# Performance work log

Measured on AMD Instinct MI355X. Metric: run time of the kernel, lower is better.

Reference implementation:

```python
import jax, jax.numpy as jnp
import numpy as np
from jax import lax

B, L = 16384, 32
HID, CIN = 8, 2
N_SUB = 2            # RK4 substeps per spline interval (fixed-step stand-in for torchcde's adaptive solver)
T10_LO, T10_HI = 0.1, 7.0


def push_zeros(a):
    # torch: move nonzero entries of each row to the right end, zeros to the left.
    # stable ascending sort on validity key (0 for zeros, 1 for valid) reproduces this exactly
    # because the invalid entries are exactly 0.
    keys = (a != 0).astype(jnp.int32)
    order = jnp.argsort(keys, axis=1)  # jax sorts are stable
    return jnp.take_along_axis(a, order, axis=1)


def setup_inputs() -> dict:
    key = jax.random.key(0)
    ks = jax.random.split(key, 12)
    fa_len = jax.random.randint(ks[0], (B, 1), L // 2, L + 1)          # 16..32 valid points
    valid = jnp.arange(L)[None, :] < fa_len                             # (B, L)
    X_fa_in = jnp.where(valid, jax.random.uniform(ks[1], (B, L), minval=0.1, maxval=1.1), 0.0)
    fa_vals_in = jnp.where(valid, jax.random.uniform(ks[2], (B, L), minval=0.05, maxval=0.45), 0.0)
    TR_vals = jax.random.uniform(ks[3], (B, 1), minval=0.003, maxval=0.01)
    fa_mask = valid

    def lin(k, fout, fin):
        kw, kb = jax.random.split(k)
        s = 1.0 / np.sqrt(fin)
        return (jax.random.uniform(kw, (fout, fin), minval=-s, maxval=s),
                jax.random.uniform(kb, (fout,), minval=-s, maxval=s))

    W_init, b_init = lin(ks[4], HID, CIN)        # self.initial: Linear(2, 8)
    W1, b1 = lin(ks[5], 256, HID)                # CDE_Func.linear1
    W2, b2 = lin(ks[6], CIN * HID, 256)          # CDE_Func.linear2
    Wr1, br1 = lin(ks[7], 200, HID)              # reg_T10
    Wr2, br2 = lin(ks[8], 200, 200)
    Wr3, br3 = lin(ks[9], 1, 200)
    return dict(X_fa_in=X_fa_in, fa_vals_in=fa_vals_in, TR_vals=TR_vals,
                W_init=W_init, b_init=b_init, W1=W1, b1=b1, W2=W2, b2=b2,
                Wr1=Wr1, br1=br1, Wr2=Wr2, br2=br2, Wr3=Wr3, br3=br3,
                fa_mask=fa_mask, fa_len=fa_len)


def _forward(X_fa_in, fa_vals_in, TR_vals, W_init, b_init, W1, b1, W2, b2,
             Wr1, br1, Wr2, br2, Wr3, br3, fa_mask, fa_len):
    fl = fa_len[:, 0]                       # (B,) int
    fl_f = fl.astype(X_fa_in.dtype)
    mean = jnp.sum(X_fa_in, axis=1) / fl_f
    Xn = X_fa_in / mean[:, None]
    X_fa = push_zeros(Xn)
    fa_vals = push_zeros(fa_vals_in)
    bidx = jnp.arange(X_fa.shape[0])
    last_X = X_fa[bidx, fl - 1][:, None]            # pushed array indexed at fa_len-1 (as in torch)
    last_fa = fa_vals_in[bidx, fl - 1][:, None]     # original array indexed at fa_len-1
    X_fa = jnp.where(X_fa == 0.0, last_X, X_fa)
    fa_vals = jnp.where(fa_vals == 0.0, last_fa, fa_vals)
    x = jnp.stack([fa_vals, X_fa], axis=-1)         # (B, L, 2): channels (fa, X)

    # Hermite cubic with backward differences, unit knot spacing t_i = i
    diffs = x[:, 1:] - x[:, :-1]                    # (B, L-1, C)
    m = jnp.concatenate([diffs[:, :1], diffs], axis=1)  # m_0 = fwd diff, m_i = backward diff
    X0s, X1s = x[:, :-1], x[:, 1:]                  # per-interval knot values (B, L-1, C)
    M0s, M1s = m[:, :-1], m[:, 1:]

    z0 = x[:, 0] @ W_init.T + b_init                # X.evaluate(interval[0]) == first knot

    def f(z):  # CDE vector field: (B, HID) -> (B, HID, CIN)
        h = jax.nn.relu(z @ W1.T + b1)
        g = jnp.tanh(h @ W2.T + b2)
        return g.reshape(z.shape[0], HID, CIN)

    hstep = 1.0 / N_SUB
    nI = x.shape[1] - 1
    intervals = jnp.repeat(jnp.arange(nI), N_SUB)
    s0s = jnp.tile(jnp.arange(N_SUB) * hstep, nI).astype(x.dtype)

    def step(z, ts):
        i, s0 = ts
        x0, x1 = X0s[:, i], X1s[:, i]
        m0, m1 = M0s[:, i], M1s[:, i]

        def dX(s):  # spline derivative dX/dt at local coord s in [0,1]
            s2 = s * s
            return ((6 * s2 - 6 * s) * x0 + (3 * s2 - 4 * s + 1) * m0 +
                    (-6 * s2 + 6 * s) * x1 + (3 * s2 - 2 * s) * m1)

        def F(s, zz):
            return jnp.einsum('bhc,bc->bh', f(zz), dX(s))

        k1 = F(s0, z)
        k2 = F(s0 + hstep / 2, z + 0.5 * hstep * k1)
        k3 = F(s0 + hstep / 2, z + 0.5 * hstep * k2)
        k4 = F(s0 + hstep, z + hstep * k3)
        return z + (hstep / 6) * (k1 + 2 * k2 + 2 * k3 + k4), None

    z_T, _ = lax.scan(step, z0, (intervals, s0s))

    h1 = jax.nn.gelu(z_T @ Wr1.T + br1, approximate=False)
    h2 = jax.nn.gelu(h1 @ Wr2.T + br2, approximate=False)
    t = (h2 @ Wr3.T + br3)[:, 0]
    T10 = T10_LO + jax.nn.sigmoid(t)[:, None] * (T10_HI - T10_LO)   # (B, 1)
    R1 = 1.0 / T10
    E = jnp.exp(-TR_vals * R1)                                      # (B, 1)
    X_out = (1 - E) * jnp.sin(fa_vals_in) / (1 - jnp.cos(fa_vals_in) * E)
    mean2 = jnp.sum(X_out, axis=1) / fl_f
    X_out = X_out / mean2[:, None]
    M0 = jnp.ones_like(T10)
    return X_out, T10, M0


def reference(X_fa_in, fa_vals_in, TR_vals, W_init, b_init, W1, b1, W2, b2,
              Wr1, br1, Wr2, br2, Wr3, br3, fa_mask, fa_len):
    return _forward(X_fa_in, fa_vals_in, TR_vals, W_init, b_init, W1, b1, W2, b2,
                    Wr1, br1, Wr2, br2, Wr3, br3, fa_mask, fa_len)
```

## Files before the change

kernel.cpp:

```cpp
#include <hip/hip_runtime.h>
#include <hip/hip_bf16.h>

#define B_ROWS 16384
#define L_SEQ  32

typedef _Float16 f16;
typedef __attribute__((ext_vector_type(8))) _Float16 f16x8;
typedef __attribute__((ext_vector_type(4))) float f32x4;
typedef __attribute__((ext_vector_type(4))) unsigned int u32x4;

__device__ __forceinline__ unsigned pkh(float a, float b) {
    return __builtin_bit_cast(unsigned, __builtin_amdgcn_cvt_pkrtz(a, b));
}
__device__ __forceinline__ float tanh_fast(float x) {
    float e = __expf(2.0f * x);
    float r = __builtin_amdgcn_rcpf(e + 1.0f);
    return fmaf(-2.0f, r, 1.0f);
}
__device__ __forceinline__ float gelu_exact(float x) {
    return 0.5f * x * (1.0f + erff(x * 0.70710678118654752440f));
}

__global__ __launch_bounds__(256, 1) void ode_kernel(
    const float* __restrict__ Xin, const float* __restrict__ Fin,
    const int*   __restrict__ fa_len,
    const float* __restrict__ Wi,  const float* __restrict__ bi,
    const float* __restrict__ W1g, const float* __restrict__ b1g,
    const float* __restrict__ W2g, const float* __restrict__ b2g,
    float* __restrict__ zT)
{
    __shared__ __align__(16) float xm[64 * 132];
#define XM(r_, i_, c_) xm[(r_) * 132 + (i_) * 4 + (c_)]

    const int tid = threadIdx.x;
    const int g16 = tid >> 4, sub = tid & 15;

    float mean_r[4]; int fl_r[4];
#pragma unroll
    for (int r = 0; r < 4; ++r) {
        const int row_l = g16 * 4 + r;
        const int row   = blockIdx.x * 64 + row_l;
        const float* Xr = Xin + row * L_SEQ;
        const float* Fr = Fin + row * L_SEQ;
        float xr0 = Xr[sub], xr1 = Xr[sub + 16];
        float fr0 = Fr[sub], fr1 = Fr[sub + 16];
        fl_r[r] = fa_len[row];
        float s = xr0 + xr1;
        s += __shfl_xor(s, 1, 16);
        s += __shfl_xor(s, 2, 16);
        s += __shfl_xor(s, 4, 16);
        s += __shfl_xor(s, 8, 16);
        mean_r[r] = s / (float)fl_r[r];
        XM(row_l, sub, 0)      = fr0; XM(row_l, sub, 1)      = xr0;
        XM(row_l, sub + 16, 0) = fr1; XM(row_l, sub + 16, 1) = xr1;
    }
    __syncthreads();

    float ff[4][2], xf[4][2];
#pragma unroll
    for (int r = 0; r < 4; ++r) {
        const int row_l = g16 * 4 + r;
        const int fl = fl_r[r];
        const float mean = mean_r[r];
        const int shift = L_SEQ - fl;
        int lsrc  = fl - 1 - shift;
        int lsrcC = lsrc < 0 ? 0 : lsrc;
        float lastX = (lsrc >= 0) ? (XM(row_l, lsrcC, 1) / mean) : 0.0f;
        float lastF = XM(row_l, fl - 1, 0);
#pragma unroll
        for (int u = 0; u < 2; ++u) {
            int p = sub + u * 16;
            int src = p - shift;
            int sc  = src < 0 ? 0 : src;
            float fraw = XM(row_l, sc, 0);
            float xraw = XM(row_l, sc, 1);
            ff[r][u] = (src >= 0) ? fraw : lastF;
            xf[r][u] = (src >= 0) ? (xraw / mean) : lastX;
        }
    }
    __syncthreads();
#pragma unroll
    for (int r = 0; r < 4; ++r) {
        const int row_l = g16 * 4 + r;
#pragma unroll
        for (int u = 0; u < 2; ++u) {
            int p = sub + u * 16;
            XM(row_l, p, 0) = ff[r][u];
            XM(row_l, p, 1) = xf[r][u];
        }
    }
    __syncthreads();
#pragma unroll
    for (int r = 0; r < 4; ++r) {
        const int row_l = g16 * 4 + r;
#pragma unroll
        for (int u = 0; u < 2; ++u) {
            int p = sub + u * 16;
            int qd = (p == 0) ? 1 : p;
            XM(row_l, p, 2) = XM(row_l, qd, 0) - XM(row_l, qd - 1, 0);
            XM(row_l, p, 3) = XM(row_l, qd, 1) - XM(row_l, qd - 1, 1);
        }
    }
    __syncthreads();

    const int wv   = tid >> 6;
    const int lane = tid & 63;
    const int n    = lane & 15;
    const int q    = lane >> 4;
    const int rowl = wv * 16 + n;
    const int rowg = blockIdx.x * 64 + rowl;

    u32x4 a1[16];
#pragma unroll
    for (int t = 0; t < 16; ++t) {
        const float* wr = W1g + (t * 16 + n) * 8 + (q < 2 ? q * 4 : 0);
        float4 w4 = *(const float4*)wr;
        float b1v = b1g[t * 16 + n];
        unsigned d0 = (q < 2) ? pkh(w4.x, w4.y) : (q == 2 ? pkh(b1v, 0.0f) : 0u);
        unsigned d1 = (q < 2) ? pkh(w4.z, w4.w) : 0u;
        a1[t] = (u32x4){d0, d1, 0u, 0u};
    }
    u32x4 a2[8];
#pragma unroll
    for (int kk = 0; kk < 8; ++kk) {
        const float* w2r = W2g + n * 256 + kk * 32 + 4 * q;
        float4 p0 = *(const float4*)(w2r);
        float4 p1 = *(const float4*)(w2r + 16);
        a2[kk] = (u32x4){pkh(p0.x, p0.y), pkh(p0.z, p0.w), pkh(p1.x, p1.y), pkh(p1.z, p1.w)};
    }
    f32x4 c2seed;
#pragma unroll
    for (int r = 0; r < 4; ++r) c2seed[r] = b2g[4 * q + r];

    float f0 = XM(rowl, 0, 0), X0 = XM(rowl, 0, 1);
    float z0 = fmaf(Wi[(2 * q) * 2], f0, fmaf(Wi[(2 * q) * 2 + 1], X0, bi[2 * q]));
    float z1 = fmaf(Wi[(2 * q + 1) * 2], f0, fmaf(Wi[(2 * q + 1) * 2 + 1], X0, bi[2 * q + 1]));

    const int bpi = (((q & 1) << 5) + n) << 2;
    const f32x4 zero4 = {0.f, 0.f, 0.f, 0.f};

    auto FEVAL = [&](float zza, float zzb, float d0c, float d1c, float& ko0, float& ko1) {
        unsigned myz = pkh(zza, zzb);
        int b0 = __builtin_amdgcn_ds_bpermute(bpi, (int)myz);
        int b1 = __builtin_amdgcn_ds_bpermute(bpi + 64, (int)myz);
        unsigned bz0 = (q < 2) ? (unsigned)b0 : (q == 2 ? 0x3C00u : 0u);
        unsigned bz1 = (q < 2) ? (unsigned)b1 : 0u;
        f16x8 bz = __builtin_bit_cast(f16x8, (u32x4){bz0, bz1, 0u, 0u});

        f32x4 c1[16];
#pragma unroll
        for (int t = 0; t < 16; ++t)
            c1[t] = __builtin_amdgcn_mfma_f32_16x16x32_f16(
                __builtin_bit_cast(f16x8, a1[t]), bz, zero4, 0, 0, 0);

        u32x4 hf[8];
#pragma unroll
        for (int kk = 0; kk < 8; ++kk) {
            float v0 = fmaxf(c1[2 * kk][0], 0.f),     v1 = fmaxf(c1[2 * kk][1], 0.f);
            float v2 = fmaxf(c1[2 * kk][2], 0.f),     v3 = fmaxf(c1[2 * kk][3], 0.f);
            float w0 = fmaxf(c1[2 * kk + 1][0], 0.f), w1 = fmaxf(c1[2 * kk + 1][1], 0.f);
            float w2 = fmaxf(c1[2 * kk + 1][2], 0.f), w3 = fmaxf(c1[2 * kk + 1][3], 0.f);
            hf[kk] = (u32x4){pkh(v0, v1), pkh(v2, v3), pkh(w0, w1), pkh(w2, w3)};
        }

        f32x4 c2a = c2seed, c2b = zero4;
#pragma unroll
        for (int kk = 0; kk < 4; ++kk) {
            c2a = __builtin_amdgcn_mfma_f32_16x16x32_f16(
                __builtin_bit_cast(f16x8, a2[kk]), __builtin_bit_cast(f16x8, hf[kk]), c2a, 0, 0, 0);
            c2b = __builtin_amdgcn_mfma_f32_16x16x32_f16(
                __builtin_bit_cast(f16x8, a2[kk + 4]), __builtin_bit_cast(f16x8, hf[kk + 4]), c2b, 0, 0, 0);
        }
        f32x4 G = c2a + c2b;

        float t0 = tanh_fast(G[0]), t1 = tanh_fast(G[1]);
        float t2 = tanh_fast(G[2]), t3 = tanh_fast(G[3]);
        ko0 = fmaf(t0, d0c, t1 * d1c);
        ko1 = fmaf(t2, d0c, t3 * d1c);
    };

#pragma unroll 1
    for (int i = 0; i < 31; ++i) {
        float4 P0 = *(const float4*)&XM(rowl, i, 0);
        float4 P1 = *(const float4*)&XM(rowl, i + 1, 0);
        float m0f = P0.z, m0X = P0.w, m1f = P1.z, m1X = P1.w;
        float df  = P0.x - P1.x, dXx = P0.y - P1.y;

        float d25f = fmaf(-1.125f, df,  fmaf(0.1875f, m0f, -0.3125f * m1f));
        float d25X = fmaf(-1.125f, dXx, fmaf(0.1875f, m0X, -0.3125f * m1X));
        float d50f = fmaf(-1.5f,   df,  fmaf(-0.25f,  m0f, -0.25f   * m1f));
        float d50X = fmaf(-1.5f,   dXx, fmaf(-0.25f,  m0X, -0.25f   * m1X));
        float d75f = fmaf(-1.125f, df,  fmaf(-0.3125f, m0f, 0.1875f * m1f));
        float d75X = fmaf(-1.125f, dXx, fmaf(-0.3125f, m0X, 0.1875f * m1X));

#pragma unroll 1
        for (int ssi = 0; ssi < 2; ++ssi) {
            float daf = ssi ? d50f : m0f,  daX = ssi ? d50X : m0X;
            float dbf = ssi ? d75f : d25f, dbX = ssi ? d75X : d25X;
            float ddf = ssi ? m1f  : d50f, ddX = ssi ? m1X  : d50X;

            float k1a, k1b, k2a, k2b, k3a, k3b, k4a, k4b, zza, zzb;
            FEVAL(z0, z1, daf, daX, k1a, k1b);
            zza = fmaf(0.25f, k1a, z0); zzb = fmaf(0.25f, k1b, z1);
            FEVAL(zza, zzb, dbf, dbX, k2a, k2b);
            zza = fmaf(0.25f, k2a, z0); zzb = fmaf(0.25f, k2b, z1);
            FEVAL(zza, zzb, dbf, dbX, k3a, k3b);
            zza = fmaf(0.5f, k3a, z0);  zzb = fmaf(0.5f, k3b, z1);
            FEVAL(zza, zzb, ddf, ddX, k4a, k4b);

            float ka = fmaf(2.f, k2a, k1a); ka = fmaf(2.f, k3a, ka);
            float kb = fmaf(2.f, k2b, k1b); kb = fmaf(2.f, k3b, kb);
            z0 = fmaf(1.f / 12.f, ka + k4a, z0);
            z1 = fmaf(1.f / 12.f, kb + k4b, z1);
        }
    }

    *(float2*)(zT + rowg * 8 + 2 * q) = make_float2(z0, z1);
#undef XM
}

__global__ __launch_bounds__(256) void readout_kernel(
    const float* __restrict__ zT,
    const float* __restrict__ Fin,
    const float* __restrict__ TRv,
    const int*   __restrict__ fa_len,
    const float* __restrict__ Wr1, const float* __restrict__ br1,
    const float* __restrict__ Wr2, const float* __restrict__ br2,
    const float* __restrict__ Wr3, const float* __restrict__ br3,
    float* __restrict__ out)
{
    __shared__ float h1s[32][200];
    __shared__ float w2s[40][200];
    const int tid = threadIdx.x;
    const int g = tid >> 3, sub = tid & 7;
    const int row = blockIdx.x * 32 + g;

    float4 za = *(const float4*)(zT + row * 8);
    float4 zb = *(const float4*)(zT + row * 8 + 4);

#pragma unroll 5
    for (int t = 0; t < 25; ++t) {
        int j = sub + 8 * t;
        const float* w = Wr1 + j * 8;
        float4 wa = *(const float4*)(w);
        float4 wb = *(const float4*)(w + 4);
        float acc = br1[j];
        acc = fmaf(wa.x, za.x, acc);
        acc = fmaf(wa.y, za.y, acc);
        acc = fmaf(wa.z, za.z, acc);
        acc = fmaf(wa.w, za.w, acc);
        acc = fmaf(wb.x, zb.x, acc);
        acc = fmaf(wb.y, zb.y, acc);
        acc = fmaf(wb.z, zb.z, acc);
        acc = fmaf(wb.w, zb.w, acc);
        h1s[g][j] = gelu_exact(acc);
    }
    __syncthreads();

    float tacc = 0.0f;
    for (int c = 0; c < 5; ++c) {
        const float4* src4 = (const float4*)(Wr2 + c * 8000);
        float4* dst4 = (float4*)(&w2s[0][0]);
#pragma unroll
        for (int it = 0; it < 8; ++it) {
            int idx = tid + it * 256;
            if (idx < 2000) dst4[idx] = src4[idx];
        }
        __syncthreads();
#pragma unroll
        for (int t = 0; t < 5; ++t) {
            int ol = sub + 8 * t;
            int o  = c * 40 + ol;
            float acc = br2[o];
            const float4* wvv = (const float4*)(&w2s[ol][0]);
            const float4* hv = (const float4*)(&h1s[g][0]);
#pragma unroll 10
            for (int qq = 0; qq < 50; ++qq) {
                float4 a = wvv[qq], b = hv[qq];
                acc = fmaf(a.x, b.x, acc);
                acc = fmaf(a.y, b.y, acc);
                acc = fmaf(a.z, b.z, acc);
                acc = fmaf(a.w, b.w, acc);
            }
            float h2 = gelu_exact(acc);
            tacc = fmaf(Wr3[o], h2, tacc);
        }
        __syncthreads();
    }

    tacc += __shfl_xor(tacc, 1, 8);
    tacc += __shfl_xor(tacc, 2, 8);
    tacc += __shfl_xor(tacc, 4, 8);
    float tval = tacc + br3[0];
    float sig  = __fdividef(1.0f, 1.0f + __expf(-tval));
    float T10  = 0.1f + 6.9f * sig;
    float R1   = 1.0f / T10;
    float E    = __expf(-TRv[row] * R1);

    float xo[4]; float ssum = 0.f;
#pragma unroll
    for (int t = 0; t < 4; ++t) {
        int p = sub + 8 * t;
        float fa = Fin[row * 32 + p];
        float sn = __sinf(fa), cs = __cosf(fa);
        float v = __fdividef((1.0f - E) * sn, 1.0f - cs * E);
        xo[t] = v; ssum += v;
    }
    ssum += __shfl_xor(ssum, 1, 8);
    ssum += __shfl_xor(ssum, 2, 8);
    ssum += __shfl_xor(ssum, 4, 8);
    float mean2 = ssum / (float)fa_len[row];
    float inv   = __fdividef(1.0f, mean2);
#pragma unroll
    for (int t = 0; t < 4; ++t) {
        int p = sub + 8 * t;
        out[row * 32 + p] = xo[t] * inv;
    }
    if (sub == 0) {
        out[B_ROWS * L_SEQ + row] = T10;
        out[B_ROWS * L_SEQ + B_ROWS + row] = 1.0f;
    }
}

extern "C" void kernel_launch(void* const* d_in, const int* in_sizes, int n_in,
                              void* d_out, int out_size, void* d_ws, size_t ws_size,
                              hipStream_t stream) {
    const float* Xin  = (const float*)d_in[0];
    const float* Fin  = (const float*)d_in[1];
    const float* TRv  = (const float*)d_in[2];
    const float* Wi   = (const float*)d_in[3];
    const float* bi   = (const float*)d_in[4];
    const float* W1g  = (const float*)d_in[5];
    const float* b1g  = (const float*)d_in[6];
    const float* W2g  = (const float*)d_in[7];
    const float* b2g  = (const float*)d_in[8];
    const float* Wr1  = (const float*)d_in[9];
    const float* br1  = (const float*)d_in[10];
    const float* Wr2  = (const float*)d_in[11];
    const float* br2  = (const float*)d_in[12];
    const float* Wr3  = (const float*)d_in[13];
    const float* br3  = (const float*)d_in[14];
    const int*   flen = (const int*)d_in[16];

    float* outp = (float*)d_out;
    float* zT   = (float*)d_ws;

    ode_kernel<<<dim3(B_ROWS / 64), dim3(256), 0, stream>>>(
        Xin, Fin, flen, Wi, bi, W1g, b1g, W2g, b2g, zT);
    readout_kernel<<<dim3(B_ROWS / 32), dim3(256), 0, stream>>>(
        zT, Fin, TRv, flen, Wr1, br1, Wr2, br2, Wr3, br3, outp);
}
```

Measured before the change: 304.7 us.

## Move readout MLP onto f16 MFMA and pin ODE weight fragments in VGPRs

The readout kernel is rewritten so the 8→200 and 200→200 layers run as 16x16x32 f16 MFMAs with 64 rows per block, in place of scalar FP32 dot products through LDS. Wr2 fragments are loaded straight from global memory for each tile. In the ODE kernel, the ReLU now runs as a packed f16 max after conversion, and empty asm constraints keep the weight fragments resident in registers. This trades FP32 accuracy in the readout head for f16 precision and relies on L2 caching of Wr2.

```diff
diff --git a/kernel.cpp b/kernel.cpp
--- a/kernel.cpp
+++ b/kernel.cpp
@@ -19,6 +19,11 @@
 }
 __device__ __forceinline__ float gelu_exact(float x) {
     return 0.5f * x * (1.0f + erff(x * 0.70710678118654752440f));
+}
+__device__ __forceinline__ void pin4(u32x4& v) {
+    unsigned x0 = v[0], x1 = v[1], x2 = v[2], x3 = v[3];
+    asm volatile("" : "+v"(x0), "+v"(x1), "+v"(x2), "+v"(x3));
+    v = (u32x4){x0, x1, x2, x3};
 }
 
 __global__ __launch_bounds__(256, 1) void ode_kernel(
@@ -119,6 +124,7 @@
         unsigned d0 = (q < 2) ? pkh(w4.x, w4.y) : (q == 2 ? pkh(b1v, 0.0f) : 0u);
         unsigned d1 = (q < 2) ? pkh(w4.z, w4.w) : 0u;
         a1[t] = (u32x4){d0, d1, 0u, 0u};
+        pin4(a1[t]);
     }
     u32x4 a2[8];
 #pragma unroll
@@ -127,6 +133,7 @@
         float4 p0 = *(const float4*)(w2r);
         float4 p1 = *(const float4*)(w2r + 16);
         a2[kk] = (u32x4){pkh(p0.x, p0.y), pkh(p0.z, p0.w), pkh(p1.x, p1.y), pkh(p1.z, p1.w)};
+        pin4(a2[kk]);
     }
     f32x4 c2seed;
 #pragma unroll
@@ -138,6 +145,7 @@
 
     const int bpi = (((q & 1) << 5) + n) << 2;
     const f32x4 zero4 = {0.f, 0.f, 0.f, 0.f};
+    const f16x8 zf16 = {0, 0, 0, 0, 0, 0, 0, 0};
 
     auto FEVAL = [&](float zza, float zzb, float d0c, float d1c, float& ko0, float& ko1) {
         unsigned myz = pkh(zza, zzb);
@@ -153,23 +161,23 @@
             c1[t] = __builtin_amdgcn_mfma_f32_16x16x32_f16(
                 __builtin_bit_cast(f16x8, a1[t]), bz, zero4, 0, 0, 0);
 
-        u32x4 hf[8];
+        f16x8 hf[8];
 #pragma unroll
         for (int kk = 0; kk < 8; ++kk) {
-            float v0 = fmaxf(c1[2 * kk][0], 0.f),     v1 = fmaxf(c1[2 * kk][1], 0.f);
-            float v2 = fmaxf(c1[2 * kk][2], 0.f),     v3 = fmaxf(c1[2 * kk][3], 0.f);
-            float w0 = fmaxf(c1[2 * kk + 1][0], 0.f), w1 = fmaxf(c1[2 * kk + 1][1], 0.f);
-            float w2 = fmaxf(c1[2 * kk + 1][2], 0.f), w3 = fmaxf(c1[2 * kk + 1][3], 0.f);
-            hf[kk] = (u32x4){pkh(v0, v1), pkh(v2, v3), pkh(w0, w1), pkh(w2, w3)};
+            u32x4 w = (u32x4){pkh(c1[2 * kk][0],     c1[2 * kk][1]),
+                              pkh(c1[2 * kk][2],     c1[2 * kk][3]),
+                              pkh(c1[2 * kk + 1][0], c1[2 * kk + 1][1]),
+                              pkh(c1[2 * kk + 1][2], c1[2 * kk + 1][3])};
+            hf[kk] = __builtin_elementwise_max(__builtin_bit_cast(f16x8, w), zf16);
         }
 
         f32x4 c2a = c2seed, c2b = zero4;
 #pragma unroll
         for (int kk = 0; kk < 4; ++kk) {
             c2a = __builtin_amdgcn_mfma_f32_16x16x32_f16(
-                __builtin_bit_cast(f16x8, a2[kk]), __builtin_bit_cast(f16x8, hf[kk]), c2a, 0, 0, 0);
+                __builtin_bit_cast(f16x8, a2[kk]), hf[kk], c2a, 0, 0, 0);
             c2b = __builtin_amdgcn_mfma_f32_16x16x32_f16(
-                __builtin_bit_cast(f16x8, a2[kk + 4]), __builtin_bit_cast(f16x8, hf[kk + 4]), c2b, 0, 0, 0);
+                __builtin_bit_cast(f16x8, a2[kk + 4]), hf[kk + 4], c2b, 0, 0, 0);
         }
         f32x4 G = c2a + c2b;
 
@@ -219,7 +227,7 @@
 #undef XM
 }
 
-__global__ __launch_bounds__(256) void readout_kernel(
+__global__ __launch_bounds__(256, 1) void readout_kernel(
     const float* __restrict__ zT,
     const float* __restrict__ Fin,
     const float* __restrict__ TRv,
@@ -229,96 +237,118 @@
     const float* __restrict__ Wr3, const float* __restrict__ br3,
     float* __restrict__ out)
 {
-    __shared__ float h1s[32][200];
-    __shared__ float w2s[40][200];
-    const int tid = threadIdx.x;
-    const int g = tid >> 3, sub = tid & 7;
-    const int row = blockIdx.x * 32 + g;
-
-    float4 za = *(const float4*)(zT + row * 8);
-    float4 zb = *(const float4*)(zT + row * 8 + 4);
-
-#pragma unroll 5
-    for (int t = 0; t < 25; ++t) {
-        int j = sub + 8 * t;
-        const float* w = Wr1 + j * 8;
-        float4 wa = *(const float4*)(w);
-        float4 wb = *(const float4*)(w + 4);
-        float acc = br1[j];
-        acc = fmaf(wa.x, za.x, acc);
-        acc = fmaf(wa.y, za.y, acc);
-        acc = fmaf(wa.z, za.z, acc);
-        acc = fmaf(wa.w, za.w, acc);
-        acc = fmaf(wb.x, zb.x, acc);
-        acc = fmaf(wb.y, zb.y, acc);
-        acc = fmaf(wb.z, zb.z, acc);
-        acc = fmaf(wb.w, zb.w, acc);
-        h1s[g][j] = gelu_exact(acc);
-    }
-    __syncthreads();
-
-    float tacc = 0.0f;
-    for (int c = 0; c < 5; ++c) {
-        const float4* src4 = (const float4*)(Wr2 + c * 8000);
-        float4* dst4 = (float4*)(&w2s[0][0]);
-#pragma unroll
-        for (int it = 0; it < 8; ++it) {
-            int idx = tid + it * 256;
-            if (idx < 2000) dst4[idx] = src4[idx];
-        }
-        __syncthreads();
-#pragma unroll
-        for (int t = 0; t < 5; ++t) {
-            int ol = sub + 8 * t;
-            int o  = c * 40 + ol;
-            float acc = br2[o];
-            const float4* wvv = (const float4*)(&w2s[ol][0]);
-            const float4* hv = (const float4*)(&h1s[g][0]);
-#pragma unroll 10
-            for (int qq = 0; qq < 50; ++qq) {
-                float4 a = wvv[qq], b = hv[qq];
-                acc = fmaf(a.x, b.x, acc);
-                acc = fmaf(a.y, b.y, acc);
-                acc = fmaf(a.z, b.z, acc);
-                acc = fmaf(a.w, b.w, acc);
+    const int tid  = threadIdx.x;
+    const int wv   = tid >> 6;
+    const int lane = tid & 63;
+    const int n    = lane & 15;
+    const int q    = lane >> 4;
+    const int rowg = blockIdx.x * 64 + wv * 16 + n;
+
+    const f32x4 zero4 = {0.f, 0.f, 0.f, 0.f};
+
+    u32x4 bzw = {0u, 0u, 0u, 0u};
+    if (q < 2) {
+        float4 z4 = *(const float4*)(zT + rowg * 8 + 4 * q);
+        bzw[0] = pkh(z4.x, z4.y);
+        bzw[1] = pkh(z4.z, z4.w);
+    } else if (q == 2) {
+        bzw[0] = 0x3C00u;
+    }
+    f16x8 bz = __builtin_bit_cast(f16x8, bzw);
+
+    f32x4 c1[13];
+#pragma unroll
+    for (int t = 0; t < 13; ++t) {
+        int m = 16 * t + n;
+        u32x4 af = {0u, 0u, 0u, 0u};
+        if (q < 2) {
+            if (m < 200) {
+                float4 w4 = *(const float4*)(Wr1 + m * 8 + 4 * q);
+                af[0] = pkh(w4.x, w4.y);
+                af[1] = pkh(w4.z, w4.w);
             }
-            float h2 = gelu_exact(acc);
-            tacc = fmaf(Wr3[o], h2, tacc);
-        }
-        __syncthreads();
-    }
-
-    tacc += __shfl_xor(tacc, 1, 8);
-    tacc += __shfl_xor(tacc, 2, 8);
-    tacc += __shfl_xor(tacc, 4, 8);
-    float tval = tacc + br3[0];
+        } else if (q == 2) {
+            float b = (m < 200) ? br1[m] : 0.0f;
+            af[0] = pkh(b, 0.0f);
+        }
+        c1[t] = __builtin_amdgcn_mfma_f32_16x16x32_f16(
+            __builtin_bit_cast(f16x8, af), bz, zero4, 0, 0, 0);
+    }
+
+    f16x8 hf[7];
+#pragma unroll
+    for (int kk = 0; kk < 7; ++kk) {
+        float g0 = gelu_exact(c1[2 * kk][0]), g1 = gelu_exact(c1[2 * kk][1]);
+        float g2 = gelu_exact(c1[2 * kk][2]), g3 = gelu_exact(c1[2 * kk][3]);
+        float g4 = 0.f, g5 = 0.f, g6 = 0.f, g7 = 0.f;
+        if (kk < 6) {
+            g4 = gelu_exact(c1[2 * kk + 1][0]); g5 = gelu_exact(c1[2 * kk + 1][1]);
+            g6 = gelu_exact(c1[2 * kk + 1][2]); g7 = gelu_exact(c1[2 * kk + 1][3]);
+        }
+        u32x4 w = (u32x4){pkh(g0, g1), pkh(g2, g3), pkh(g4, g5), pkh(g6, g7)};
+        hf[kk] = __builtin_bit_cast(f16x8, w);
+    }
+
+    float tpart = 0.0f;
+#pragma unroll 1
+    for (int mt = 0; mt < 13; ++mt) {
+        int mb = 16 * mt + 4 * q;
+        f32x4 c2 = zero4;
+        if (mb + 3 < 200) c2 = *(const f32x4*)(br2 + mb);
+        int m2 = 16 * mt + n;
+#pragma unroll
+        for (int kk = 0; kk < 7; ++kk) {
+            u32x4 af = {0u, 0u, 0u, 0u};
+            if (m2 < 200) {
+                int k0 = 32 * kk + 4 * q;
+                const float* wr = Wr2 + m2 * 200 + k0;
+                if (k0 + 3 < 200) {
+                    float4 wa = *(const float4*)(wr);
+                    af[0] = pkh(wa.x, wa.y); af[1] = pkh(wa.z, wa.w);
+                }
+                if (k0 + 19 < 200) {
+                    float4 wb = *(const float4*)(wr + 16);
+                    af[2] = pkh(wb.x, wb.y); af[3] = pkh(wb.z, wb.w);
+                }
+            }
+            c2 = __builtin_amdgcn_mfma_f32_16x16x32_f16(
+                __builtin_bit_cast(f16x8, af), hf[kk], c2, 0, 0, 0);
+        }
+        float4 w3 = make_float4(0.f, 0.f, 0.f, 0.f);
+        if (mb + 3 < 200) w3 = *(const float4*)(Wr3 + mb);
+        tpart = fmaf(w3.x, gelu_exact(c2[0]), tpart);
+        tpart = fmaf(w3.y, gelu_exact(c2[1]), tpart);
+        tpart = fmaf(w3.z, gelu_exact(c2[2]), tpart);
+        tpart = fmaf(w3.w, gelu_exact(c2[3]), tpart);
+    }
+    tpart += __shfl_xor(tpart, 16);
+    tpart += __shfl_xor(tpart, 32);
+
+    float tval = tpart + br3[0];
     float sig  = __fdividef(1.0f, 1.0f + __expf(-tval));
     float T10  = 0.1f + 6.9f * sig;
-    float R1   = 1.0f / T10;
-    float E    = __expf(-TRv[row] * R1);
-
-    float xo[4]; float ssum = 0.f;
-#pragma unroll
-    for (int t = 0; t < 4; ++t) {
-        int p = sub + 8 * t;
-        float fa = Fin[row * 32 + p];
+    float E    = __expf(-TRv[rowg] * __builtin_amdgcn_rcpf(T10));
+
+    const float* Fr = Fin + rowg * 32 + 8 * q;
+    float xo[8]; float ssum = 0.0f;
+#pragma unroll
+    for (int j = 0; j < 8; ++j) {
+        float fa = Fr[j];
         float sn = __sinf(fa), cs = __cosf(fa);
         float v = __fdividef((1.0f - E) * sn, 1.0f - cs * E);
-        xo[t] = v; ssum += v;
-    }
-    ssum += __shfl_xor(ssum, 1, 8);
-    ssum += __shfl_xor(ssum, 2, 8);
-    ssum += __shfl_xor(ssum, 4, 8);
-    float mean2 = ssum / (float)fa_len[row];
+        xo[j] = v; ssum += v;
+    }
+    ssum += __shfl_xor(ssum, 16);
+    ssum += __shfl_xor(ssum, 32);
+    float mean2 = ssum / (float)fa_len[rowg];
     float inv   = __fdividef(1.0f, mean2);
-#pragma unroll
-    for (int t = 0; t < 4; ++t) {
-        int p = sub + 8 * t;
-        out[row * 32 + p] = xo[t] * inv;
-    }
-    if (sub == 0) {
-        out[B_ROWS * L_SEQ + row] = T10;
-        out[B_ROWS * L_SEQ + B_ROWS + row] = 1.0f;
+
+    float4* dst = (float4*)(out + rowg * 32 + 8 * q);
+    dst[0] = make_float4(xo[0] * inv, xo[1] * inv, xo[2] * inv, xo[3] * inv);
+    dst[1] = make_float4(xo[4] * inv, xo[5] * inv, xo[6] * inv, xo[7] * inv);
+    if (q == 0) {
+        out[B_ROWS * L_SEQ + rowg] = T10;
+        out[B_ROWS * L_SEQ + B_ROWS + rowg] = 1.0f;
     }
 }
 
@@ -347,6 +377,6 @@
 
     ode_kernel<<<dim3(B_ROWS / 64), dim3(256), 0, stream>>>(
         Xin, Fin, flen, Wi, bi, W1g, b1g, W2g, b2g, zT);
-    readout_kernel<<<dim3(B_ROWS / 32), dim3(256), 0, stream>>>(
+    readout_kernel<<<dim3(B_ROWS / 64), dim3(256), 0, stream>>>(
         zT, Fin, TRv, flen, Wr1, br1, Wr2, br2, Wr3, br3, outp);
 }
```

New measurement: 273.5 us. -10.2%, faster.
